# Kernel tuning notes

Hardware: AMD Instinct MI355X
Metric: run time of the kernel (lower is better)

## Reference

```python
import jax, jax.numpy as jnp
import numpy as np

N, E, IN_DIM, H, OUT, MAPD = 20000, 640000, 24, 128, 24, 512
SLOPE = 0.01  # torch F.leaky_relu default


def setup_inputs() -> dict:
    key = jax.random.key(0)
    ks = jax.random.split(key, 20)
    g = lambda i, shape, s: jax.random.normal(ks[i], shape, jnp.float32) * s
    inp = {
        "feats": g(0, (N, IN_DIM), 1.0),
        "e_w": jax.random.uniform(ks[1], (E, 1), dtype=jnp.float32),
        "maps_embedding": g(2, (N, MAPD), 1.0),
        "snorm_n": jnp.ones((N, 1), jnp.float32),
        "src": jax.random.randint(ks[3], (E,), 0, N),
        "dst": jax.random.randint(ks[4], (E,), 0, N),
        "W_eh": g(5, (H, IN_DIM), (2.0 / IN_DIM) ** 0.5), "b_eh": jnp.zeros((H,), jnp.float32),
        "W_ee": g(6, (H, 1), 1.0), "b_ee": jnp.zeros((H,), jnp.float32),
        "W_cat": g(7, (H, H + MAPD), (2.0 / (H + MAPD)) ** 0.5), "b_cat": jnp.zeros((H,), jnp.float32),
        "Ws1": g(8, (H, H), (2.0 / H) ** 0.5), "Wf1": g(9, (H, H), (2.0 / H) ** 0.5),
        "a1": g(10, (2 * H,), (2.0 / (2 * H)) ** 0.5),
        "Ws2": g(11, (H, H), (2.0 / H) ** 0.5), "Wf2": g(12, (H, H), (2.0 / H) ** 0.5),
        "a2": g(13, (2 * H,), (2.0 / (2 * H)) ** 0.5),
        "W_out": g(14, (OUT, H), (2.0 / H) ** 0.5), "b_out": jnp.zeros((OUT,), jnp.float32),
    }
    return inp


def gat_layer(h, src, dst, Ws, Wf, a):
    # My_GATLayer with (as constructed in My_GAT) relu=False, att_ew=False, dropouts=0.
    h_in = h
    h_s = h @ Ws.T                         # [N,H] self transform
    z = h @ Wf.T                           # [N,H] message transform
    # attention score = leaky_relu(a^T [z_src, z_dst]) computed via per-node halves
    s_src = z @ a[:H]                      # [N]
    s_dst = z @ a[H:]                      # [N]
    e = jax.nn.leaky_relu(s_src[src] + s_dst[dst], SLOPE)          # [E]
    # numerically stable segment softmax over incoming edges grouped by dst
    m = jax.ops.segment_max(e, dst, num_segments=N)
    m = jnp.where(jnp.isfinite(m), m, 0.0)
    ex = jnp.exp(e - m[dst])
    denom = jax.ops.segment_sum(ex, dst, num_segments=N)
    alpha = ex / jnp.maximum(denom[dst], 1e-16)                    # [E]
    agg = jax.ops.segment_sum(alpha[:, None] * z[src], dst, num_segments=N)  # [N,H]
    indeg = jax.ops.segment_sum(jnp.ones_like(e), dst, num_segments=N)
    # DGL update_all leaves zero-in-degree nodes at their prior ndata['h'] (= h_in)
    h_node = jnp.where(indeg[:, None] > 0, h_s + agg, h_in)
    return h_in + h_node                   # residual connection; relu disabled (positional-arg bug)


def reference(feats, e_w, maps_embedding, snorm_n, src, dst,
              W_eh, b_eh, W_ee, b_ee, W_cat, b_cat,
              Ws1, Wf1, a1, Ws2, Wf2, a2, W_out, b_out):
    feats = feats.reshape(feats.shape[0], -1)
    h = feats @ W_eh.T + b_eh                                  # embedding_h
    _e = e_w @ W_ee.T + b_ee                                   # edge embedding (stored on g.edata['w'], unused since att_ew binds to attn_drop)
    h = jnp.concatenate([maps_embedding, h], axis=-1) @ W_cat.T + b_cat
    h = jax.nn.relu(h)
    h = gat_layer(h, src, dst, Ws1, Wf1, a1)
    h = gat_layer(h, src, dst, Ws2, Wf2, a2)
    return h @ W_out.T + b_out
```

## Files before the change

kernel.cpp:

```cpp
#include <hip/hip_runtime.h>

#define HBLK 128
#define EPB 4096

typedef __attribute__((ext_vector_type(8))) short s8v;
typedef __attribute__((ext_vector_type(4))) float f32x4;
typedef __attribute__((ext_vector_type(8))) _Float16 h8f;

__device__ inline void split2(float x, short& h, short& l) {
    unsigned hb = __float_as_uint(x) & 0xFFFF0000u;
    float hf = __uint_as_float(hb);
    float lf = x - hf;
    h = (short)(hb >> 16);
    l = (short)(__float_as_uint(lf) >> 16);
}

__device__ inline void split8(const float4& a0, const float4& a1, s8v& ah, s8v& al) {
    float vv[8];
    *(float4*)&vv[0] = a0;
    *(float4*)&vv[4] = a1;
#pragma unroll
    for (int e = 0; e < 8; ++e) {
        short hh, ll;
        split2(vv[e], hh, ll);
        ah[e] = hh;
        al[e] = ll;
    }
}


__global__ void bin_hist(const int* __restrict__ dst, int* __restrict__ histT,
                         int E, int NB1) {
    __shared__ int h[256];
    const int t = threadIdx.x, blk = blockIdx.x;
    h[t] = 0;
    __syncthreads();
    const int e0 = blk * EPB;
    const int e1 = min(E, e0 + EPB);
    for (int e = e0 + t; e < e1; e += 256)
        atomicAdd(&h[dst[e] >> 7], 1);
    __syncthreads();
    histT[t * NB1 + blk] = h[t];
}

__global__ void scan1(const int* __restrict__ counts, int* __restrict__ offs,
                      int* __restrict__ bsums, int n) {
    __shared__ int lds[256];
    const int t = threadIdx.x;
    const int i = blockIdx.x * 256 + t;
    const int v = (i < n) ? counts[i] : 0;
    lds[t] = v;
    __syncthreads();
    for (int off = 1; off < 256; off <<= 1) {
        int add = (t >= off) ? lds[t - off] : 0;
        __syncthreads();
        lds[t] += add;
        __syncthreads();
    }
    if (i < n) offs[i] = lds[t] - v;
    if (t == 255) bsums[blockIdx.x] = lds[255];
}

__global__ void scan2(int* __restrict__ bsums, int nb) {
    __shared__ int lds[256];
    const int t = threadIdx.x;
    const int v = (t < nb) ? bsums[t] : 0;
    lds[t] = v;
    __syncthreads();
    for (int off = 1; off < 256; off <<= 1) {
        int add = (t >= off) ? lds[t - off] : 0;
        __syncthreads();
        lds[t] += add;
        __syncthreads();
    }
    if (t < nb) bsums[t] = lds[t] - v;
}

__global__ void bin_scatter(const int* __restrict__ src, const int* __restrict__ dst,
                            const int* __restrict__ histT, const int* __restrict__ bsums,
                            int2* __restrict__ ebuf, int E, int NB1) {
    __shared__ int cur[256];
    const int t = threadIdx.x, blk = blockIdx.x;
    const int li = t * NB1 + blk;
    cur[t] = histT[li] + bsums[li >> 8];
    __syncthreads();
    const int e0 = blk * EPB;
    const int e1 = min(E, e0 + EPB);
    for (int e = e0 + t; e < e1; e += 256) {
        const int d = dst[e];
        const int p = atomicAdd(&cur[d >> 7], 1);
        ebuf[p] = make_int2(src[e], d);
    }
}

__global__ void bucket_sort(const int2* __restrict__ ebuf, const int* __restrict__ histT,
                            const int* __restrict__ bsums,
                            int* __restrict__ offs, int* __restrict__ srcs,
                            int N, int E, int NB1) {
    __shared__ int cnt[256];
    __shared__ int cur[256];
    const int t = threadIdx.x, b = blockIdx.x;
    const int li0 = b * NB1;
    const int ebase = histT[li0] + bsums[li0 >> 8];
    int eend = E;
    if (b + 1 < 256) {
        const int li1 = (b + 1) * NB1;
        eend = histT[li1] + bsums[li1 >> 8];
    }
    cnt[t] = 0;
    __syncthreads();
    for (int e = ebase + t; e < eend; e += 256)
        atomicAdd(&cnt[ebuf[e].y & 127], 1);
    __syncthreads();
    const int own = cnt[t];
    for (int off = 1; off < 256; off <<= 1) {
        int add = (t >= off) ? cnt[t - off] : 0;
        __syncthreads();
        cnt[t] += add;
        __syncthreads();
    }
    const int excl = cnt[t] - own;
    cur[t] = ebase + excl;
    const int node = (b << 7) + t;
    if (t < 128 && node < N) offs[node] = ebase + excl;
    if (b == 0 && t == 0) offs[N] = E;
    __syncthreads();
    for (int e = ebase + t; e < eend; e += 256) {
        const int2 ed = ebuf[e];
        const int p = atomicAdd(&cur[ed.y & 127], 1);
        srcs[p] = ed.x;
    }
}

__global__ void pack_wcat(const float* __restrict__ Wcat, int ldw, int mapd,
                          const float* __restrict__ Weh, int indim,
                          const float* __restrict__ beh, const float* __restrict__ bcat,
                          short* __restrict__ dh, short* __restrict__ dl,
                          float* __restrict__ bcomb, int K) {
    const long i = (long)blockIdx.x * 256 + threadIdx.x;
    const long total = (long)HBLK * K;
    if (i < total) {
        const int c = (int)(i / K), k = (int)(i % K);
        float x = 0.f;
        if (k < mapd) {
            x = Wcat[(long)c * ldw + k];
        } else if (k < mapd + indim) {
            const float* wc = Wcat + (long)c * ldw + mapd;
            const int kk = k - mapd;
            float s = 0.f;
            for (int j = 0; j < HBLK; ++j) s += wc[j] * Weh[j * indim + kk];
            x = s;
        }
        short h, l;
        split2(x, h, l);
        const int j = c >> 4, l16 = c & 15;
        const int chunk = k >> 5, quad = (k >> 3) & 3, t = k & 7;
        const long off = (((long)(chunk * 8 + j) * 64) + quad * 16 + l16) * 8 + t;
        dh[off] = h;
        dl[off] = l;
    } else if (i < total + HBLK) {
        const int c = (int)(i - total);
        const float* wc = Wcat + (long)c * ldw + mapd;
        float s = bcat[c];
        for (int j = 0; j < HBLK; ++j) s += wc[j] * beh[j];
        bcomb[c] = s;
    }
}

__global__ void split_w_packA(const float* __restrict__ W0, const float* __restrict__ W1,
                              const float* __restrict__ W2, const float* __restrict__ W3,
                              const float* __restrict__ Wout, int outd,
                              short* __restrict__ dh, short* __restrict__ dl,
                              short* __restrict__ doh, short* __restrict__ dol) {
    const int m = blockIdx.y;
    const long i = (long)blockIdx.x * 256 + threadIdx.x;
    if (m < 4) {
        const float* Ws[4] = {W0, W1, W2, W3};
        const int c = (int)(i >> 7), k = (int)(i & 127);
        float x = Ws[m][c * HBLK + k];
        short h, l;
        split2(x, h, l);
        const int j = c >> 4, l16 = c & 15;
        const int chunk = k >> 5, quad = (k >> 3) & 3, t = k & 7;
        const long off = (long)m * 16384 + (((long)(chunk * 8 + j) * 64) + quad * 16 + l16) * 8 + t;
        dh[off] = h;
        dl[off] = l;
    } else {
        if (i >= 32 * HBLK) return;
        const int c = (int)(i >> 7), k = (int)(i & 127);
        float x = (c < outd) ? Wout[c * HBLK + k] : 0.f;
        short h, l;
        split2(x, h, l);
        const int j = c >> 4, l16 = c & 15;
        const int chunk = k >> 5, quad = (k >> 3) & 3, t = k & 7;
        const long off = (((long)(chunk * 2 + j) * 64) + quad * 16 + l16) * 8 + t;
        doh[off] = h;
        dol[off] = l;
    }
}

__global__ __launch_bounds__(256, 2) void gemm_bigk(
    const float* __restrict__ A1, int lda1, int K1,
    const float* __restrict__ A2, int lda2, int Kin,
    int K,
    const short* __restrict__ Wh, const short* __restrict__ Wl,
    const float* __restrict__ bias,
    float* __restrict__ Cf, int M)
{
    __shared__ short lds_h[2][4096];
    __shared__ short lds_l[2][4096];
    const int tid = threadIdx.x;
    const int wv = tid >> 6;
    const int lane = tid & 63;
    const int l16 = lane & 15;
    const int quad = lane >> 4;
    const int m0 = blockIdx.x * 64 + wv * 16;
    int ra = m0 + l16;
    if (ra >= M) ra = M - 1;
    const long r1 = (long)ra * lda1;
    const long r2 = (long)ra * lda2;
    const int NC = K >> 5;

    f32x4 acc[8];
#pragma unroll
    for (int j = 0; j < 8; ++j) acc[j] = (f32x4){0.f, 0.f, 0.f, 0.f};

#define LOAD_A(d0, d1, kb)                                      \
    {                                                           \
        const int col0 = (kb) + quad * 8;                       \
        if (col0 < K1) {                                        \
            const float* ap = A1 + r1 + col0;                   \
            d0 = *(const float4*)ap;                            \
            d1 = *(const float4*)(ap + 4);                      \
        } else if (col0 < Kin) {                                \
            const float* ap = A2 + r2 + (col0 - K1);            \
            d0 = *(const float4*)ap;                            \
            d1 = *(const float4*)(ap + 4);                      \
        } else {                                                \
            d0 = make_float4(0.f, 0.f, 0.f, 0.f);               \
            d1 = make_float4(0.f, 0.f, 0.f, 0.f);               \
        }                                                       \
    }
#define LOAD_W(r0, r1w, r2w, r3, c)                             \
    {                                                           \
        const int4* gh = (const int4*)(Wh + (long)(c) * 4096);  \
        const int4* gl = (const int4*)(Wl + (long)(c) * 4096);  \
        r0 = gh[tid * 2]; r1w = gh[tid * 2 + 1];                \
        r2w = gl[tid * 2]; r3 = gl[tid * 2 + 1];                \
    }
#define WRITE_W(b, r0, r1w, r2w, r3)                            \
    {                                                           \
        int4* bh = (int4*)lds_h[b];                             \
        int4* bl = (int4*)lds_l[b];                             \
        bh[tid * 2] = r0; bh[tid * 2 + 1] = r1w;                \
        bl[tid * 2] = r2w; bl[tid * 2 + 1] = r3;                \
    }

    int4 wa0, wa1, wa2, wa3, wb0, wb1, wb2, wb3;
    LOAD_W(wa0, wa1, wa2, wa3, 0)
    WRITE_W(0, wa0, wa1, wa2, wa3)
    LOAD_W(wa0, wa1, wa2, wa3, 1)
    LOAD_W(wb0, wb1, wb2, wb3, 2)
    float4 a0c, a1c, a0n, a1n, a0p, a1p;
    float4 a0q = make_float4(0.f, 0.f, 0.f, 0.f);
    float4 a1q = make_float4(0.f, 0.f, 0.f, 0.f);
    LOAD_A(a0c, a1c, 0)
    LOAD_A(a0n, a1n, 32)
    LOAD_A(a0p, a1p, 64)
    asm volatile("s_waitcnt lgkmcnt(0)" ::: "memory");
    __builtin_amdgcn_s_barrier();
    asm volatile("" ::: "memory");

    for (int c = 0; c < NC; ++c) {
        const int nb = c & 1;
        if (c + 3 < NC) {
            LOAD_A(a0q, a1q, (c + 3) * 32)
        }
        s8v ah, al;
        split8(a0c, a1c, ah, al);
#pragma unroll
        for (int j = 0; j < 8; ++j) {
            const s8v whf = *(const s8v*)&lds_h[nb][(j * 64 + lane) * 8];
            const s8v wlf = *(const s8v*)&lds_l[nb][(j * 64 + lane) * 8];
            acc[j] = __builtin_amdgcn_mfma_f32_16x16x32_bf16(ah, whf, acc[j], 0, 0, 0);
            acc[j] = __builtin_amdgcn_mfma_f32_16x16x32_bf16(ah, wlf, acc[j], 0, 0, 0);
            acc[j] = __builtin_amdgcn_mfma_f32_16x16x32_bf16(al, whf, acc[j], 0, 0, 0);
        }
        if (c + 1 < NC) {
            WRITE_W(nb ^ 1, wa0, wa1, wa2, wa3)
            wa0 = wb0; wa1 = wb1; wa2 = wb2; wa3 = wb3;
            if (c + 3 < NC) LOAD_W(wb0, wb1, wb2, wb3, c + 3)
            asm volatile("s_waitcnt lgkmcnt(0)" ::: "memory");
            __builtin_amdgcn_s_barrier();
            asm volatile("" ::: "memory");
        }
        a0c = a0n; a1c = a1n;
        a0n = a0p; a1n = a1p;
        a0p = a0q; a1p = a1q;
    }
#undef LOAD_A
#undef LOAD_W
#undef WRITE_W

#pragma unroll
    for (int r = 0; r < 4; ++r) {
        const int gr = m0 + quad * 4 + r;
        if (gr >= M) continue;
#pragma unroll
        for (int j = 0; j < 8; ++j) {
            const int col = j * 16 + l16;
            float v = acc[j][r] + bias[col];
            Cf[(long)gr * HBLK + col] = fmaxf(v, 0.f);
        }
    }
}

__global__ __launch_bounds__(256, 2) void gemm_smallk(
    const float* __restrict__ A,
    const short* __restrict__ W1h, const short* __restrict__ W1l,
    const short* __restrict__ W2h, const short* __restrict__ W2l,
    float* __restrict__ C1f, _Float16* __restrict__ Czh,
    const float* __restrict__ avec,
    float* __restrict__ sOut, float* __restrict__ dOut, int M)
{
    __shared__ short lh[16384];
    __shared__ short ll[16384];
    const short* __restrict__ Wh = blockIdx.y ? W2h : W1h;
    const short* __restrict__ Wl = blockIdx.y ? W2l : W1l;
    float* __restrict__ Cf = blockIdx.y ? nullptr : C1f;
    _Float16* __restrict__ Ch16 = blockIdx.y ? Czh : nullptr;
    const float* __restrict__ av = blockIdx.y ? avec : nullptr;
    const int tid = threadIdx.x;
    const int wv = tid >> 6;
    const int lane = tid & 63;
    const int l16 = lane & 15;
    const int quad = lane >> 4;
    const int m0 = blockIdx.x * 64 + wv * 16;
    int ra = m0 + l16;
    if (ra >= M) ra = M - 1;
    const float* arow = A + (long)ra * HBLK + quad * 8;

    {
        const int4* gh = (const int4*)Wh;
        const int4* gl = (const int4*)Wl;
        int4* bh = (int4*)lh;
        int4* bl = (int4*)ll;
#pragma unroll
        for (int i = 0; i < 8; ++i) {
            bh[i * 256 + tid] = gh[i * 256 + tid];
            bl[i * 256 + tid] = gl[i * 256 + tid];
        }
    }
    float4 aw0[4], aw1[4];
#pragma unroll
    for (int c = 0; c < 4; ++c) {
        aw0[c] = *(const float4*)(arow + c * 32);
        aw1[c] = *(const float4*)(arow + c * 32 + 4);
    }
    f32x4 acc[8];
#pragma unroll
    for (int j = 0; j < 8; ++j) acc[j] = (f32x4){0.f, 0.f, 0.f, 0.f};
    __syncthreads();

#pragma unroll
    for (int c = 0; c < 4; ++c) {
        s8v ah, al;
        split8(aw0[c], aw1[c], ah, al);
#pragma unroll
        for (int j = 0; j < 8; ++j) {
            const s8v whf = *(const s8v*)&lh[((c * 8 + j) * 64 + lane) * 8];
            const s8v wlf = *(const s8v*)&ll[((c * 8 + j) * 64 + lane) * 8];
            acc[j] = __builtin_amdgcn_mfma_f32_16x16x32_bf16(ah, whf, acc[j], 0, 0, 0);
            acc[j] = __builtin_amdgcn_mfma_f32_16x16x32_bf16(ah, wlf, acc[j], 0, 0, 0);
            acc[j] = __builtin_amdgcn_mfma_f32_16x16x32_bf16(al, whf, acc[j], 0, 0, 0);
        }
    }

#pragma unroll
    for (int r = 0; r < 4; ++r) {
        const int gr = m0 + quad * 4 + r;
        if (gr >= M) continue;
#pragma unroll
        for (int j = 0; j < 8; ++j) {
            const int col = j * 16 + l16;
            const float v = acc[j][r];
            if (Cf) Cf[(long)gr * HBLK + col] = v;
            if (Ch16) Ch16[(long)gr * HBLK + col] = (_Float16)v;
        }
    }

    if (av) {
        float av0[8], av1[8];
#pragma unroll
        for (int j = 0; j < 8; ++j) {
            av0[j] = av[j * 16 + l16];
            av1[j] = av[128 + j * 16 + l16];
        }
#pragma unroll
        for (int r = 0; r < 4; ++r) {
            float ssp = 0.f, sdp = 0.f;
#pragma unroll
            for (int j = 0; j < 8; ++j) {
                const float v = acc[j][r];
                ssp += v * av0[j];
                sdp += v * av1[j];
            }
#pragma unroll
            for (int off = 1; off < 16; off <<= 1) {
                ssp += __shfl_xor(ssp, off);
                sdp += __shfl_xor(sdp, off);
            }
            const int gr = m0 + quad * 4 + r;
            if (l16 == 0 && gr < M) {
                sOut[gr] = ssp;
                dOut[gr] = sdp;
            }
        }
    }
}

__global__ __launch_bounds__(256) void gemm_out(
    const float* __restrict__ A,
    const short* __restrict__ Wh, const short* __restrict__ Wl,
    const float* __restrict__ bias, float* __restrict__ out,
    int M, int OUTD)
{
    __shared__ short lh[4096], ll[4096];
    const int tid = threadIdx.x;
    {
        const int4* gh = (const int4*)Wh;
        const int4* gl = (const int4*)Wl;
        int4* bh = (int4*)lh;
        int4* bl = (int4*)ll;
        bh[tid * 2] = gh[tid * 2];
        bh[tid * 2 + 1] = gh[tid * 2 + 1];
        bl[tid * 2] = gl[tid * 2];
        bl[tid * 2 + 1] = gl[tid * 2 + 1];
    }
    const int wv = tid >> 6;
    const int lane = tid & 63;
    const int l16 = lane & 15;
    const int quad = lane >> 4;
    const int m0 = blockIdx.x * 64 + wv * 16;
    int ra = m0 + l16;
    if (ra >= M) ra = M - 1;
    const float* arow = A + (long)ra * HBLK + quad * 8;

    f32x4 acc[2];
    acc[0] = (f32x4){0.f, 0.f, 0.f, 0.f};
    acc[1] = (f32x4){0.f, 0.f, 0.f, 0.f};
    __syncthreads();

#pragma unroll
    for (int c = 0; c < 4; ++c) {
        const float4 a0 = *(const float4*)(arow + c * 32);
        const float4 a1 = *(const float4*)(arow + c * 32 + 4);
        s8v ah, al;
        split8(a0, a1, ah, al);
#pragma unroll
        for (int j = 0; j < 2; ++j) {
            const s8v whf = *(const s8v*)&lh[((c * 2 + j) * 64 + lane) * 8];
            const s8v wlf = *(const s8v*)&ll[((c * 2 + j) * 64 + lane) * 8];
            acc[j] = __builtin_amdgcn_mfma_f32_16x16x32_bf16(ah, whf, acc[j], 0, 0, 0);
            acc[j] = __builtin_amdgcn_mfma_f32_16x16x32_bf16(ah, wlf, acc[j], 0, 0, 0);
            acc[j] = __builtin_amdgcn_mfma_f32_16x16x32_bf16(al, whf, acc[j], 0, 0, 0);
        }
    }

#pragma unroll
    for (int r = 0; r < 4; ++r) {
        const int gr = m0 + quad * 4 + r;
        if (gr >= M) continue;
#pragma unroll
        for (int j = 0; j < 2; ++j) {
            const int col = j * 16 + l16;
            if (col < OUTD)
                out[(long)gr * OUTD + col] = acc[j][r] + bias[col];
        }
    }
}

__global__ void gat_gather(const float* __restrict__ h_in, const float* __restrict__ hs,
                           const _Float16* __restrict__ zh,
                           const float* __restrict__ s_src, const float* __restrict__ s_dst,
                           const int* __restrict__ offs, const int* __restrict__ srcs,
                           float* __restrict__ h_out, int N) {
    const int wave = threadIdx.x >> 6;
    const int lane = threadIdx.x & 63;
    const int n = blockIdx.x * 4 + wave;
    if (n >= N) return;
    const int g = lane >> 4, l = lane & 15;
    const int beg = offs[n], end = offs[n + 1];

    float acc[8] = {};
    if (end > beg) {
        const float sd = s_dst[n];
        float m = -INFINITY, s = 0.f;
        for (int i = beg + lane; i < end; i += 64) {
            float e = sd + s_src[srcs[i]];
            e = e > 0.f ? e : 0.01f * e;
            float nm = fmaxf(m, e);
            s = s * __expf(m - nm) + __expf(e - nm);
            m = nm;
        }
#pragma unroll
        for (int off = 32; off > 0; off >>= 1) {
            float m2 = __shfl_down(m, off);
            float s2 = __shfl_down(s, off);
            if (m2 > m) {
                float t = m; m = m2; m2 = t;
                float ts = s; s = s2; s2 = ts;
            }
            s = (m == -INFINITY) ? 0.f : s + s2 * __expf(m2 - m);
        }
        m = __shfl(m, 0);
        s = __shfl(s, 0);
        const float inv = 1.f / fmaxf(s, 1e-16f);

        int i = beg + g;
        for (; i + 12 < end; i += 16) {
            const int s0 = srcs[i];
            const int s1 = srcs[i + 4];
            const int s2i = srcs[i + 8];
            const int s3 = srcs[i + 12];
            float e0 = sd + s_src[s0];
            float e1 = sd + s_src[s1];
            float e2 = sd + s_src[s2i];
            float e3 = sd + s_src[s3];
            e0 = e0 > 0.f ? e0 : 0.01f * e0;
            e1 = e1 > 0.f ? e1 : 0.01f * e1;
            e2 = e2 > 0.f ? e2 : 0.01f * e2;
            e3 = e3 > 0.f ? e3 : 0.01f * e3;
            const float w0 = __expf(e0 - m) * inv;
            const float w1 = __expf(e1 - m) * inv;
            const float w2 = __expf(e2 - m) * inv;
            const float w3 = __expf(e3 - m) * inv;
            const h8f z0 = *(const h8f*)(zh + (long)s0 * HBLK + 8 * l);
            const h8f z1 = *(const h8f*)(zh + (long)s1 * HBLK + 8 * l);
            const h8f z2 = *(const h8f*)(zh + (long)s2i * HBLK + 8 * l);
            const h8f z3 = *(const h8f*)(zh + (long)s3 * HBLK + 8 * l);
#pragma unroll
            for (int e = 0; e < 8; ++e)
                acc[e] += w0 * (float)z0[e] + w1 * (float)z1[e]
                        + w2 * (float)z2[e] + w3 * (float)z3[e];
        }
        for (; i < end; i += 4) {
            const int s0 = srcs[i];
            float e0 = sd + s_src[s0];
            e0 = e0 > 0.f ? e0 : 0.01f * e0;
            const float w0 = __expf(e0 - m) * inv;
            const h8f z0 = *(const h8f*)(zh + (long)s0 * HBLK + 8 * l);
#pragma unroll
            for (int e = 0; e < 8; ++e)
                acc[e] += w0 * (float)z0[e];
        }
#pragma unroll
        for (int e = 0; e < 8; ++e) {
            acc[e] += __shfl_down(acc[e], 32);
            acc[e] += __shfl_down(acc[e], 16);
        }
    }

    if (g == 0) {
        const long base = (long)n * HBLK + 8 * l;
        const float4 hi0 = *(const float4*)(h_in + base);
        const float4 hi1 = *(const float4*)(h_in + base + 4);
        float o[8];
        if (end > beg) {
            const float4 hv0 = *(const float4*)(hs + base);
            const float4 hv1 = *(const float4*)(hs + base + 4);
            const float* hip = (const float*)&hi0;
            const float* hvp = (const float*)&hv0;
#pragma unroll
            for (int e = 0; e < 4; ++e) o[e] = hip[e] + hvp[e] + acc[e];
            const float* hip1 = (const float*)&hi1;
            const float* hvp1 = (const float*)&hv1;
#pragma unroll
            for (int e = 0; e < 4; ++e) o[4 + e] = hip1[e] + hvp1[e] + acc[4 + e];
        } else {
            const float* hip = (const float*)&hi0;
            const float* hip1 = (const float*)&hi1;
#pragma unroll
            for (int e = 0; e < 4; ++e) o[e] = 2.f * hip[e];
#pragma unroll
            for (int e = 0; e < 4; ++e) o[4 + e] = 2.f * hip1[e];
        }
        *(float4*)(h_out + base) = *(float4*)&o[0];
        *(float4*)(h_out + base + 4) = *(float4*)&o[4];
    }
}

extern "C" void kernel_launch(void* const* d_in, const int* in_sizes, int n_in,
                              void* d_out, int out_size, void* d_ws, size_t ws_size,
                              hipStream_t stream) {
    const float* feats = (const float*)d_in[0];
    const float* maps  = (const float*)d_in[2];
    const int* src = (const int*)d_in[4];
    const int* dst = (const int*)d_in[5];
    const float* W_eh  = (const float*)d_in[6];
    const float* b_eh  = (const float*)d_in[7];
    const float* W_cat = (const float*)d_in[10];
    const float* b_cat = (const float*)d_in[11];
    const float* Ws1 = (const float*)d_in[12];
    const float* Wf1 = (const float*)d_in[13];
    const float* a1  = (const float*)d_in[14];
    const float* Ws2 = (const float*)d_in[15];
    const float* Wf2 = (const float*)d_in[16];
    const float* a2  = (const float*)d_in[17];
    const float* W_out = (const float*)d_in[18];
    const float* b_out = (const float*)d_in[19];

    const int N = in_sizes[3];
    const int E = in_sizes[4];
    const int IN_DIM = in_sizes[0] / N;
    const int MAPD = in_sizes[2] / N;
    const int OUTD = in_sizes[19];
    const int KCAT = MAPD + HBLK;
    const int KC = (MAPD + IN_DIM + 31) & ~31;

    char* p = (char*)d_ws;
    const size_t NH = (size_t)N * HBLK;
    float* hin  = (float*)p;  p += NH * 4;
    float* hs   = (float*)p;  p += NH * 4;
    float* hout = (float*)p;  p += NH * 4;
    _Float16* zh = (_Float16*)p; p += NH * 2;
    float* ssrc = (float*)p;  p += (size_t)N * 4;
    float* sdst = (float*)p;  p += (size_t)N * 4;
    int* offs   = (int*)p;    p += (size_t)(N + 1) * 4;
    int* srcs   = (int*)p;    p += (size_t)E * 4;
    int* bsums  = (int*)p;    p += 256 * 4;
    int* histT  = (int*)p;    p += (size_t)256 * 256 * 4;
    float* bcomb = (float*)p; p += (size_t)HBLK * 4;
    p = (char*)(((uintptr_t)p + 15) & ~(uintptr_t)15);
    int2* ebuf = (int2*)p;    p += (size_t)E * 8;
    short* Wcat_h = (short*)p; p += (size_t)HBLK * KC * 2;
    short* Wcat_l = (short*)p; p += (size_t)HBLK * KC * 2;
    short* Wout_h = (short*)p; p += (size_t)32 * HBLK * 2;
    short* Wout_l = (short*)p; p += (size_t)32 * HBLK * 2;
    short* Wly_h = (short*)p;  p += (size_t)4 * HBLK * HBLK * 2;
    short* Wly_l = (short*)p;  p += (size_t)4 * HBLK * HBLK * 2;

    const int NB1 = (E + EPB - 1) / EPB;
    const int NBUCK = (N + 127) >> 7;
    const int nHist = 256 * NB1;
    bin_hist<<<NB1, 256, 0, stream>>>(dst, histT, E, NB1);
    scan1<<<NB1, 256, 0, stream>>>(histT, histT, bsums, nHist);
    scan2<<<1, 256, 0, stream>>>(bsums, NB1);
    bin_scatter<<<NB1, 256, 0, stream>>>(src, dst, histT, bsums, ebuf, E, NB1);
    bucket_sort<<<NBUCK, 256, 0, stream>>>(ebuf, histT, bsums, offs, srcs, N, E, NB1);

    pack_wcat<<<(HBLK * KC + HBLK + 255) / 256, 256, 0, stream>>>(
        W_cat, KCAT, MAPD, W_eh, IN_DIM, b_eh, b_cat, Wcat_h, Wcat_l, bcomb, KC);
    split_w_packA<<<dim3(64, 5), 256, 0, stream>>>(
        Ws1, Wf1, Ws2, Wf2, W_out, OUTD, Wly_h, Wly_l, Wout_h, Wout_l);

    const int gGrid = (N + 63) / 64;
    const int n4 = (N + 3) / 4;

    gemm_bigk<<<gGrid, 256, 0, stream>>>(
        maps, MAPD, MAPD, feats, IN_DIM, MAPD + IN_DIM, KC,
        Wcat_h, Wcat_l, bcomb, hin, N);

    gemm_smallk<<<dim3(gGrid, 2), 256, 0, stream>>>(
        hin, Wly_h, Wly_l, Wly_h + 16384, Wly_l + 16384,
        hs, zh, a1, ssrc, sdst, N);
    gat_gather<<<n4, 256, 0, stream>>>(hin, hs, zh, ssrc, sdst, offs, srcs, hout, N);

    gemm_smallk<<<dim3(gGrid, 2), 256, 0, stream>>>(
        hout, Wly_h + 32768, Wly_l + 32768, Wly_h + 49152, Wly_l + 49152,
        hs, zh, a2, ssrc, sdst, N);
    gat_gather<<<n4, 256, 0, stream>>>(hout, hs, zh, ssrc, sdst, offs, srcs, hin, N);

    gemm_out<<<gGrid, 256, 0, stream>>>(hin, Wout_h, Wout_l, b_out, (float*)d_out, N, OUTD);
}
```

Measured before the change: 270.3 us.

## Pack edge bin entries into one int and add register-resident softmax for low-degree nodes

The binning pass now stores each edge as a single packed int (source index shifted left by 7, OR'd with the low 7 bits of dst) instead of an int2, halving ebuf traffic in bin_scatter and bucket_sort. The GAT gather kernel adds a fast path for nodes with in-degree up to 64. Each lane loads one edge's source index and score once, computes the softmax with xor-shuffle reductions, and broadcasts source and weight via shuffles. This avoids re-reading srcs and s_src and recomputing exp in a second pass. Higher-degree nodes keep the online-softmax path but lose the 4-way unrolled gather loop, and packing limits source indices to 2^24.

```diff
diff --git a/kernel.cpp b/kernel.cpp
--- a/kernel.cpp
+++ b/kernel.cpp
@@ -78,7 +78,7 @@
 
 __global__ void bin_scatter(const int* __restrict__ src, const int* __restrict__ dst,
                             const int* __restrict__ histT, const int* __restrict__ bsums,
-                            int2* __restrict__ ebuf, int E, int NB1) {
+                            int* __restrict__ ebuf, int E, int NB1) {
     __shared__ int cur[256];
     const int t = threadIdx.x, blk = blockIdx.x;
     const int li = t * NB1 + blk;
@@ -89,11 +89,11 @@
     for (int e = e0 + t; e < e1; e += 256) {
         const int d = dst[e];
         const int p = atomicAdd(&cur[d >> 7], 1);
-        ebuf[p] = make_int2(src[e], d);
-    }
-}
-
-__global__ void bucket_sort(const int2* __restrict__ ebuf, const int* __restrict__ histT,
+        ebuf[p] = (src[e] << 7) | (d & 127);
+    }
+}
+
+__global__ void bucket_sort(const int* __restrict__ ebuf, const int* __restrict__ histT,
                             const int* __restrict__ bsums,
                             int* __restrict__ offs, int* __restrict__ srcs,
                             int N, int E, int NB1) {
@@ -110,7 +110,7 @@
     cnt[t] = 0;
     __syncthreads();
     for (int e = ebase + t; e < eend; e += 256)
-        atomicAdd(&cnt[ebuf[e].y & 127], 1);
+        atomicAdd(&cnt[ebuf[e] & 127], 1);
     __syncthreads();
     const int own = cnt[t];
     for (int off = 1; off < 256; off <<= 1) {
@@ -126,9 +126,9 @@
     if (b == 0 && t == 0) offs[N] = E;
     __syncthreads();
     for (int e = ebase + t; e < eend; e += 256) {
-        const int2 ed = ebuf[e];
-        const int p = atomicAdd(&cur[ed.y & 127], 1);
-        srcs[p] = ed.x;
+        const int ed = ebuf[e];
+        const int p = atomicAdd(&cur[ed & 127], 1);
+        srcs[p] = ed >> 7;
     }
 }
 
@@ -491,73 +491,86 @@
     if (n >= N) return;
     const int g = lane >> 4, l = lane & 15;
     const int beg = offs[n], end = offs[n + 1];
+    const int deg = end - beg;
 
     float acc[8] = {};
-    if (end > beg) {
+    if (deg > 0) {
         const float sd = s_dst[n];
-        float m = -INFINITY, s = 0.f;
-        for (int i = beg + lane; i < end; i += 64) {
-            float e = sd + s_src[srcs[i]];
+        if (deg <= 64) {
+            const int sA = srcs[beg + min(lane, deg - 1)];
+            float e = sd + s_src[sA];
             e = e > 0.f ? e : 0.01f * e;
-            float nm = fmaxf(m, e);
-            s = s * __expf(m - nm) + __expf(e - nm);
-            m = nm;
-        }
-#pragma unroll
-        for (int off = 32; off > 0; off >>= 1) {
-            float m2 = __shfl_down(m, off);
-            float s2 = __shfl_down(s, off);
-            if (m2 > m) {
-                float t = m; m = m2; m2 = t;
-                float ts = s; s = s2; s2 = ts;
-            }
-            s = (m == -INFINITY) ? 0.f : s + s2 * __expf(m2 - m);
-        }
-        m = __shfl(m, 0);
-        s = __shfl(s, 0);
-        const float inv = 1.f / fmaxf(s, 1e-16f);
-
-        int i = beg + g;
-        for (; i + 12 < end; i += 16) {
-            const int s0 = srcs[i];
-            const int s1 = srcs[i + 4];
-            const int s2i = srcs[i + 8];
-            const int s3 = srcs[i + 12];
-            float e0 = sd + s_src[s0];
-            float e1 = sd + s_src[s1];
-            float e2 = sd + s_src[s2i];
-            float e3 = sd + s_src[s3];
-            e0 = e0 > 0.f ? e0 : 0.01f * e0;
-            e1 = e1 > 0.f ? e1 : 0.01f * e1;
-            e2 = e2 > 0.f ? e2 : 0.01f * e2;
-            e3 = e3 > 0.f ? e3 : 0.01f * e3;
-            const float w0 = __expf(e0 - m) * inv;
-            const float w1 = __expf(e1 - m) * inv;
-            const float w2 = __expf(e2 - m) * inv;
-            const float w3 = __expf(e3 - m) * inv;
-            const h8f z0 = *(const h8f*)(zh + (long)s0 * HBLK + 8 * l);
-            const h8f z1 = *(const h8f*)(zh + (long)s1 * HBLK + 8 * l);
-            const h8f z2 = *(const h8f*)(zh + (long)s2i * HBLK + 8 * l);
-            const h8f z3 = *(const h8f*)(zh + (long)s3 * HBLK + 8 * l);
-#pragma unroll
-            for (int e = 0; e < 8; ++e)
-                acc[e] += w0 * (float)z0[e] + w1 * (float)z1[e]
-                        + w2 * (float)z2[e] + w3 * (float)z3[e];
-        }
-        for (; i < end; i += 4) {
-            const int s0 = srcs[i];
-            float e0 = sd + s_src[s0];
-            e0 = e0 > 0.f ? e0 : 0.01f * e0;
-            const float w0 = __expf(e0 - m) * inv;
-            const h8f z0 = *(const h8f*)(zh + (long)s0 * HBLK + 8 * l);
-#pragma unroll
-            for (int e = 0; e < 8; ++e)
-                acc[e] += w0 * (float)z0[e];
-        }
-#pragma unroll
-        for (int e = 0; e < 8; ++e) {
-            acc[e] += __shfl_down(acc[e], 32);
-            acc[e] += __shfl_down(acc[e], 16);
+            if (lane >= deg) e = -INFINITY;
+            float mv = e;
+#pragma unroll
+            for (int off = 32; off; off >>= 1) mv = fmaxf(mv, __shfl_xor(mv, off));
+            const float ex = (lane < deg) ? __expf(e - mv) : 0.f;
+            float sv = ex;
+#pragma unroll
+            for (int off = 32; off; off >>= 1) sv += __shfl_xor(sv, off);
+            const float w = ex / fmaxf(sv, 1e-16f);
+
+            const int nK = (deg + 3) >> 2;
+            int k = 0;
+            for (; k + 1 < nK; k += 2) {
+                const int i0 = 4 * k + g;
+                const int i1 = i0 + 4;
+                const int s0 = __shfl(sA, i0);
+                const int s1 = __shfl(sA, i1);
+                const float w0 = __shfl(w, i0);
+                const float w1 = __shfl(w, i1);
+                const h8f z0 = *(const h8f*)(zh + (long)s0 * HBLK + 8 * l);
+                const h8f z1 = *(const h8f*)(zh + (long)s1 * HBLK + 8 * l);
+#pragma unroll
+                for (int e2 = 0; e2 < 8; ++e2)
+                    acc[e2] += w0 * (float)z0[e2] + w1 * (float)z1[e2];
+            }
+            if (k < nK) {
+                const int i0 = 4 * k + g;
+                const int s0 = __shfl(sA, i0);
+                const float w0 = __shfl(w, i0);
+                const h8f z0 = *(const h8f*)(zh + (long)s0 * HBLK + 8 * l);
+#pragma unroll
+                for (int e2 = 0; e2 < 8; ++e2)
+                    acc[e2] += w0 * (float)z0[e2];
+            }
+        } else {
+            float m = -INFINITY, s = 0.f;
+            for (int i = beg + lane; i < end; i += 64) {
+                float e = sd + s_src[srcs[i]];
+                e = e > 0.f ? e : 0.01f * e;
+                float nm = fmaxf(m, e);
+                s = s * __expf(m - nm) + __expf(e - nm);
+                m = nm;
+            }
+#pragma unroll
+            for (int off = 32; off > 0; off >>= 1) {
+                float m2 = __shfl_down(m, off);
+                float s2 = __shfl_down(s, off);
+                if (m2 > m) {
+                    float t = m; m = m2; m2 = t;
+                    float ts = s; s = s2; s2 = ts;
+                }
+                s = (m == -INFINITY) ? 0.f : s + s2 * __expf(m2 - m);
+            }
+            m = __shfl(m, 0);
+            s = __shfl(s, 0);
+            const float inv = 1.f / fmaxf(s, 1e-16f);
+            for (int i = beg + g; i < end; i += 4) {
+                const int s0 = srcs[i];
+                float e0 = sd + s_src[s0];
+                e0 = e0 > 0.f ? e0 : 0.01f * e0;
+                const float w0 = __expf(e0 - m) * inv;
+                const h8f z0 = *(const h8f*)(zh + (long)s0 * HBLK + 8 * l);
+#pragma unroll
+                for (int e2 = 0; e2 < 8; ++e2)
+                    acc[e2] += w0 * (float)z0[e2];
+            }
+        }
+#pragma unroll
+        for (int e2 = 0; e2 < 8; ++e2) {
+            acc[e2] += __shfl_down(acc[e2], 32);
+            acc[e2] += __shfl_down(acc[e2], 16);
         }
     }
 
@@ -566,7 +579,7 @@
         const float4 hi0 = *(const float4*)(h_in + base);
         const float4 hi1 = *(const float4*)(h_in + base + 4);
         float o[8];
-        if (end > beg) {
+        if (deg > 0) {
             const float4 hv0 = *(const float4*)(hs + base);
             const float4 hv1 = *(const float4*)(hs + base + 4);
             const float* hip = (const float*)&hi0;
@@ -632,7 +645,7 @@
     int* histT  = (int*)p;    p += (size_t)256 * 256 * 4;
     float* bcomb = (float*)p; p += (size_t)HBLK * 4;
     p = (char*)(((uintptr_t)p + 15) & ~(uintptr_t)15);
-    int2* ebuf = (int2*)p;    p += (size_t)E * 8;
+    int* ebuf = (int*)p;      p += (size_t)E * 4;
     short* Wcat_h = (short*)p; p += (size_t)HBLK * KC * 2;
     short* Wcat_l = (short*)p; p += (size_t)HBLK * KC * 2;
     short* Wout_h = (short*)p; p += (size_t)32 * HBLK * 2;
```

Result: faster. 260.8 us (-3.5%).
